# Kernel optimization log

Hardware: AMD Instinct MI355X
Metric: run time of the kernel (lower is better)

Reference implementation:

```python
import jax, jax.numpy as jnp
import numpy as np

BETA = 0.95
NUM_STEPS = 32


def setup_inputs() -> dict:
    key = jax.random.key(0)
    ks = jax.random.split(key, 6)
    B, IN, D, P = 1024, 512, 256, 8
    total = D * P
    x = jax.random.normal(ks[0], (B, IN), jnp.float32)
    W_proj = jax.random.normal(ks[1], (IN, total), jnp.float32) / np.sqrt(IN)
    b_proj = jnp.zeros((total,), jnp.float32)
    # uniform threshold distribution, sorted: linspace(0.5, 2.0, P)
    thresholds = jnp.linspace(0.5, 2.0, P, dtype=jnp.float32)
    rate_W = jax.random.normal(ks[2], (P, 1), jnp.float32) / np.sqrt(P)
    rate_b = jnp.zeros((1,), jnp.float32)
    conv1_w = jax.random.normal(ks[3], (P // 2, P, 3), jnp.float32) / np.sqrt(P * 3)
    conv1_b = jnp.zeros((P // 2,), jnp.float32)
    conv2_w = jax.random.normal(ks[4], (1, P // 2, 1), jnp.float32) / np.sqrt(P // 2)
    conv2_b = jnp.zeros((1,), jnp.float32)
    fusion = jnp.array([0.6, 0.4], jnp.float32)
    return dict(x=x, W_proj=W_proj, b_proj=b_proj, thresholds=thresholds,
                rate_W=rate_W, rate_b=rate_b, conv1_w=conv1_w, conv1_b=conv1_b,
                conv2_w=conv2_w, conv2_b=conv2_b, fusion=fusion)


def _conv1d(x, w, b):
    # x: [N, C_in, T], w: [C_out, C_in, K] -> [N, C_out, T] (SAME padding)
    y = jax.lax.conv_general_dilated(x, w, window_strides=(1,), padding='SAME',
                                     dimension_numbers=('NCH', 'OIH', 'NCH'))
    return y + b[None, :, None]


def reference(x, W_proj, b_proj, thresholds, rate_W, rate_b,
              conv1_w, conv1_b, conv2_w, conv2_b, fusion):
    B = x.shape[0]
    P = thresholds.shape[0]
    D = W_proj.shape[1] // P
    # constant input current per neuron: [B, D, P]
    I = (x @ W_proj + b_proj).reshape(B, D, P)

    # LIF recurrence (snntorch Leaky, reset_mechanism='subtract'):
    #   reset = H(mem_prev - thr); mem = beta*mem_prev + I - reset*thr; spk = H(mem - thr)
    def step(mem, _):
        reset = (mem > thresholds).astype(mem.dtype)
        mem = BETA * mem + I - reset * thresholds
        spk = (mem > thresholds).astype(mem.dtype)
        return mem, spk

    mem0 = jnp.zeros((B, D, P), x.dtype)
    _, spikes = jax.lax.scan(step, mem0, None, length=NUM_STEPS)  # [T, B, D, P]

    # rate branch
    rates = spikes.mean(axis=0)                        # [B, D, P]
    rate_dec = (rates @ rate_W)[..., 0] + rate_b[0]    # [B, D]

    # temporal branch: [B*D, P, T]
    s = jnp.transpose(spikes, (1, 2, 3, 0)).reshape(B * D, P, NUM_STEPS)
    h = jax.nn.relu(_conv1d(s, conv1_w, conv1_b))
    h = _conv1d(h, conv2_w, conv2_b)                   # [B*D, 1, T]
    temp_dec = h.mean(axis=-1).reshape(B, D)

    fw = jax.nn.softmax(fusion)
    return fw[0] * rate_dec + fw[1] * temp_dec
```

## Files before the change

### kernel.cpp

```cpp
#include <hip/hip_runtime.h>


constexpr int D_DIM   = 256;
constexpr int NTOT    = 2048;
constexpr int T_STEPS = 32;

typedef _Float16 f16x8 __attribute__((ext_vector_type(8)));
typedef float    f32x4 __attribute__((ext_vector_type(4)));
typedef ushort   ushort8 __attribute__((ext_vector_type(8)));

#define GLOBAL_AS __attribute__((address_space(1)))
#define LDS_AS    __attribute__((address_space(3)))

__device__ __forceinline__ void split_f16(float v, ushort& h, ushort& l) {
    const _Float16 hf = (_Float16)v;
    const _Float16 lf = (_Float16)((v - (float)hf) * 2048.0f);
    h = __builtin_bit_cast(ushort, hf);
    l = __builtin_bit_cast(ushort, lf);
}

__device__ __forceinline__ void conv_x_body(const float* __restrict__ x,
                                            ushort* __restrict__ Ah,
                                            ushort* __restrict__ Al,
                                            int blk, int t)
{
    const int idx = (blk * 256 + t) * 8;
    float v[8];
    *reinterpret_cast<float4*>(v)     = *reinterpret_cast<const float4*>(x + idx);
    *reinterpret_cast<float4*>(v + 4) = *reinterpret_cast<const float4*>(x + idx + 4);
    __align__(16) ushort h[8], l[8];
#pragma unroll
    for (int j = 0; j < 8; ++j) split_f16(v[j], h[j], l[j]);
    *reinterpret_cast<ushort8*>(Ah + idx) = *reinterpret_cast<const ushort8*>(h);
    *reinterpret_cast<ushort8*>(Al + idx) = *reinterpret_cast<const ushort8*>(l);
}

__device__ __forceinline__ void conv_w_body(const float* __restrict__ Wp,
                                            ushort* __restrict__ Bh,
                                            ushort* __restrict__ Bl,
                                            float (*tile)[69],
                                            int ib, int t)
{
    const int k0 = (ib >> 5) * 64;
    const int c0 = (ib & 31) * 64;
    {
        const int r = t >> 2, cq = (t & 3) * 16;
#pragma unroll
        for (int j = 0; j < 4; ++j)
            *reinterpret_cast<float4*>(&tile[r][cq + j * 4]) =
                *reinterpret_cast<const float4*>(Wp + (size_t)(k0 + r) * NTOT + c0 + cq + j * 4);
    }
    __syncthreads();
    const int rr = t >> 2, kc2 = (t & 3) * 16;
    __align__(16) ushort h[16], l[16];
#pragma unroll
    for (int j = 0; j < 16; ++j) split_f16(tile[kc2 + j][rr], h[j], l[j]);
    ushort* dh = Bh + (size_t)(c0 + rr) * 512 + k0 + kc2;
    ushort* dl = Bl + (size_t)(c0 + rr) * 512 + k0 + kc2;
    *reinterpret_cast<ushort8*>(dh)     = *reinterpret_cast<const ushort8*>(h);
    *reinterpret_cast<ushort8*>(dh + 8) = *reinterpret_cast<const ushort8*>(h + 8);
    *reinterpret_cast<ushort8*>(dl)     = *reinterpret_cast<const ushort8*>(l);
    *reinterpret_cast<ushort8*>(dl + 8) = *reinterpret_cast<const ushort8*>(l + 8);
}

__global__ __launch_bounds__(256)
void popcode_prep(const float* __restrict__ x, const float* __restrict__ Wp,
                  ushort* __restrict__ Ah, ushort* __restrict__ Al,
                  ushort* __restrict__ Bh, ushort* __restrict__ Bl)
{
    __shared__ float tile[64][69];
    const int t = threadIdx.x;
    if (blockIdx.x < 256) conv_x_body(x, Ah, Al, blockIdx.x, t);
    else                  conv_w_body(Wp, Bh, Bl, tile, blockIdx.x - 256, t);
}

__global__ __launch_bounds__(256)
void popcode_fused(const ushort* __restrict__ Ah_g, const ushort* __restrict__ Al_g,
                   const ushort* __restrict__ Bh_g, const ushort* __restrict__ Bl_g,
                   const float* __restrict__ bp, const float* __restrict__ thrs,
                   const float* __restrict__ rateW, const float* __restrict__ rateB,
                   const float* __restrict__ c1w, const float* __restrict__ c1b,
                   const float* __restrict__ c2w, const float* __restrict__ c2b,
                   const float* __restrict__ fus, float* __restrict__ out)
{
    __shared__ __align__(16) char smem[33664];
    LDS_AS char* lds0 = (LDS_AS char*)smem;

    const int tid  = threadIdx.x;
    const int w    = tid >> 6;
    const int lane = tid & 63;

    const int wg = ((blockIdx.x & 7) << 7) | (blockIdx.x >> 3);
    const int b0 = (wg & 15) * 64;
    const int c0 = (wg >> 4) * 32;

    const ushort* gbase = (w == 0) ? Ah_g : (w == 1) ? Al_g : (w == 2) ? Bh_g : Bl_g;
    const int     t0    = (w < 2) ? b0 : c0;
    const int     srow  = lane >> 2;
    const int     schk  = (lane & 3) * 8;
    const int     poff  = (w < 2) ? (w * 4096) : (8192 + (w - 2) * 2048);

    const int wr = (w >> 1) * 32;
    const int wc = (w & 1) * 16;
    const int lr = lane & 15;
    const int lg = lane >> 4;

    const f32x4 zero = {0.f, 0.f, 0.f, 0.f};
    f32x4 acch[2] = {zero, zero};
    f32x4 accl[2] = {zero, zero};

    auto stage = [&](int buf, int kt) {
        const int koff = kt * 32 + schk;
        const int base = buf * 12288 + poff;
        if (w < 2) {
#pragma unroll
            for (int i = 0; i < 4; ++i) {
                const ushort* src = gbase + (size_t)(t0 + srow + 16 * i) * 512 + koff;
                const int loff = __builtin_amdgcn_readfirstlane(base + i * 1024);
                __builtin_amdgcn_global_load_lds((const GLOBAL_AS uint*)src,
                                                 (LDS_AS uint*)(lds0 + loff), 16, 0, 0);
            }
        } else {
#pragma unroll
            for (int i = 0; i < 2; ++i) {
                const ushort* src = gbase + (size_t)(t0 + srow + 16 * i) * 512 + koff;
                const int loff = __builtin_amdgcn_readfirstlane(base + i * 1024);
                __builtin_amdgcn_global_load_lds((const GLOBAL_AS uint*)src,
                                                 (LDS_AS uint*)(lds0 + loff), 16, 0, 0);
            }
        }
    };

    auto compute = [&](int buf) {
        const int rbase = buf * 12288;
        f16x8 ah[2], al[2], bh, bl;
#pragma unroll
        for (int m = 0; m < 2; ++m) {
            const int row = wr + m * 16 + lr;
            ah[m] = *reinterpret_cast<const f16x8*>(smem + rbase +        row * 64 + lg * 16);
            al[m] = *reinterpret_cast<const f16x8*>(smem + rbase + 4096 + row * 64 + lg * 16);
        }
        {
            const int col = wc + lr;
            bh = *reinterpret_cast<const f16x8*>(smem + rbase +  8192 + col * 64 + lg * 16);
            bl = *reinterpret_cast<const f16x8*>(smem + rbase + 10240 + col * 64 + lg * 16);
        }
#pragma unroll
        for (int m = 0; m < 2; ++m) {
            acch[m] = __builtin_amdgcn_mfma_f32_16x16x32_f16(ah[m], bh, acch[m], 0, 0, 0);
            accl[m] = __builtin_amdgcn_mfma_f32_16x16x32_f16(al[m], bh, accl[m], 0, 0, 0);
            accl[m] = __builtin_amdgcn_mfma_f32_16x16x32_f16(ah[m], bl, accl[m], 0, 0, 0);
        }
    };

    float* wlds = (float*)(smem + 33280);
    if (tid < 96) wlds[tid] = c1w[tid];
    stage(0, 0);
    __syncthreads();

    for (int kt = 0; kt < 16; ++kt) {
        if (kt < 15) stage((kt + 1) & 1, kt + 1);
        compute(kt & 1);
        __syncthreads();
    }

    float* lutf = (float*)smem;
    for (int e = tid; e < 3072; e += 256) {
        const int k    = e >> 10;
        const int byte = (e >> 2) & 255;
        const int c    = e & 3;
        float v = (k == 1) ? c1b[c] : 0.f;
#pragma unroll
        for (int p = 0; p < 8; ++p)
            v = fmaf((float)((byte >> p) & 1), wlds[(c * 8 + p) * 3 + k], v);
        lutf[e] = v;
    }

    float* it = (float*)(smem + 24576);
    const float s = 1.0f / 2048.0f;
#pragma unroll
    for (int m = 0; m < 2; ++m)
#pragma unroll
        for (int v = 0; v < 4; ++v)
            it[(wr + m * 16 + lg * 4 + v) * 34 + wc + lr] =
                acch[m][v] + accl[m][v] * s;
    __syncthreads();

    const int row  = tid >> 2;
    const int dloc = tid & 3;
    const int dg   = (c0 >> 3) + dloc;

    const float* ip  = it + row * 34 + dloc * 8;
    float thrv[8];
#pragma unroll
    for (int p = 0; p < 8; ++p) thrv[p] = thrs[p];

    float Iv[8], mem[8];
    bool  spk[8];
    {
        const float4 bv0 = *reinterpret_cast<const float4*>(bp + dg * 8);
        const float4 bv1 = *reinterpret_cast<const float4*>(bp + dg * 8 + 4);
        Iv[0] = ip[0] + bv0.x; Iv[1] = ip[1] + bv0.y;
        Iv[2] = ip[2] + bv0.z; Iv[3] = ip[3] + bv0.w;
        Iv[4] = ip[4] + bv1.x; Iv[5] = ip[5] + bv1.y;
        Iv[6] = ip[6] + bv1.z; Iv[7] = ip[7] + bv1.w;
    }
#pragma unroll
    for (int p = 0; p < 8; ++p) { mem[p] = 0.f; spk[p] = false; }

    unsigned wrd[8] = {0u, 0u, 0u, 0u, 0u, 0u, 0u, 0u};
#pragma unroll
    for (int t = 0; t < T_STEPS; ++t) {
        unsigned by = 0u;
#pragma unroll
        for (int p = 0; p < 8; ++p) {
            const float m2 = fmaf(0.95f, mem[p], Iv[p]);
            mem[p] = spk[p] ? (m2 - thrv[p]) : m2;
            spk[p] = mem[p] > thrv[p];
            by |= spk[p] ? (1u << p) : 0u;
        }
        wrd[t >> 2] |= by << (8 * (t & 3));
    }

    float rsum = 0.f;
#pragma unroll
    for (int p = 0; p < 8; ++p) {
        const unsigned m = 0x01010101u << p;
        int cnt = 0;
#pragma unroll
        for (int q = 0; q < 8; ++q) cnt += __popc(wrd[q] & m);
        rsum = fmaf((float)cnt, rateW[p], rsum);
    }

    float w2c[4];
#pragma unroll
    for (int c = 0; c < 4; ++c) w2c[c] = c2w[c];
    auto getb = [&](int t) -> unsigned {
        return (wrd[t >> 2] >> (8 * (t & 3))) & 255u;
    };
    float tacc = 0.f;
    unsigned bprev = 0u;
    unsigned bcur  = getb(0);
#pragma unroll
    for (int t = 0; t < T_STEPS; ++t) {
        const unsigned bnext = (t < 31) ? getb(t + 1) : 0u;
        const float4 fa = *reinterpret_cast<const float4*>(lutf + bprev * 4);
        const float4 fb = *reinterpret_cast<const float4*>(lutf + 1024 + bcur * 4);
        const float4 fc = *reinterpret_cast<const float4*>(lutf + 2048 + bnext * 4);
        const float h0_ = (fa.x + fb.x) + fc.x;
        const float h1_ = (fa.y + fb.y) + fc.y;
        const float h2_ = (fa.z + fb.z) + fc.z;
        const float h3_ = (fa.w + fb.w) + fc.w;
        tacc = fmaf(fmaxf(h0_, 0.f), w2c[0], tacc);
        tacc = fmaf(fmaxf(h1_, 0.f), w2c[1], tacc);
        tacc = fmaf(fmaxf(h2_, 0.f), w2c[2], tacc);
        tacc = fmaf(fmaxf(h3_, 0.f), w2c[3], tacc);
        bprev = bcur;
        bcur  = bnext;
    }

    const float f0 = fus[0], f1 = fus[1];
    const float fm = fmaxf(f0, f1);
    const float e0 = __expf(f0 - fm), e1 = __expf(f1 - fm);
    const float inv = 1.f / (e0 + e1);

    const float rdec = rsum * (1.f / 32.f) + rateB[0];
    const float temp = tacc * (1.f / 32.f) + c2b[0];
    out[(b0 + row) * D_DIM + dg] = (e0 * inv) * rdec + (e1 * inv) * temp;
}

extern "C" void kernel_launch(void* const* d_in, const int* in_sizes, int n_in,
                              void* d_out, int out_size, void* d_ws, size_t ws_size,
                              hipStream_t stream) {
    const float* x     = (const float*)d_in[0];
    const float* Wp    = (const float*)d_in[1];
    const float* bp    = (const float*)d_in[2];
    const float* thrs  = (const float*)d_in[3];
    const float* rateW = (const float*)d_in[4];
    const float* rateB = (const float*)d_in[5];
    const float* c1w   = (const float*)d_in[6];
    const float* c1b   = (const float*)d_in[7];
    const float* c2w   = (const float*)d_in[8];
    const float* c2b   = (const float*)d_in[9];
    const float* fus   = (const float*)d_in[10];
    float* out = (float*)d_out;
    float* ws  = (float*)d_ws;

    ushort* Ah = reinterpret_cast<ushort*>(ws);
    ushort* Al = Ah + 1024 * 512;
    ushort* Bh = Al + 1024 * 512;
    ushort* Bl = Bh + 2048 * 512;

    popcode_prep<<<dim3(512), dim3(256), 0, stream>>>(x, Wp, Ah, Al, Bh, Bl);
    popcode_fused<<<dim3(1024), dim3(256), 0, stream>>>(
        Ah, Al, Bh, Bl, bp, thrs, rateW, rateB, c1w, c1b, c2w, c2b, fus, out);
}
```

Measured before the change: 122.3 us.

## Widen fused GEMM tile to 64x64 columns and halve workgroup count

Each workgroup now computes a 64x64 output tile instead of 64x32, so every wave does a 2x2 block of MFMAs and each A fragment loaded from LDS is reused across two B fragments. The staging layout changes to store MFMA-fragment-ordered chunks, so LDS reads become lane-contiguous. The LIF/decoder epilogue loops twice per thread to cover the wider tile. The grid halves to 512 blocks, which raises per-block LDS and register use and roughly doubles the serial epilogue per thread, at the cost of fewer workgroups to hide latency.

```diff
diff --git a/kernel.cpp b/kernel.cpp
--- a/kernel.cpp
+++ b/kernel.cpp
@@ -83,77 +83,68 @@
                    const float* __restrict__ c2w, const float* __restrict__ c2b,
                    const float* __restrict__ fus, float* __restrict__ out)
 {
-    __shared__ __align__(16) char smem[33664];
+    __shared__ __align__(16) char smem[49792];
     LDS_AS char* lds0 = (LDS_AS char*)smem;
 
     const int tid  = threadIdx.x;
     const int w    = tid >> 6;
     const int lane = tid & 63;
 
-    const int wg = ((blockIdx.x & 7) << 7) | (blockIdx.x >> 3);
+    const int wg = (blockIdx.x & 7) * 64 + (blockIdx.x >> 3);
     const int b0 = (wg & 15) * 64;
-    const int c0 = (wg >> 4) * 32;
+    const int c0 = (wg >> 4) * 64;
 
     const ushort* gbase = (w == 0) ? Ah_g : (w == 1) ? Al_g : (w == 2) ? Bh_g : Bl_g;
     const int     t0    = (w < 2) ? b0 : c0;
-    const int     srow  = lane >> 2;
-    const int     schk  = (lane & 3) * 8;
-    const int     poff  = (w < 2) ? (w * 4096) : (8192 + (w - 2) * 2048);
+    const int     srow  = lane & 15;
+    const int     schk  = (lane >> 4) * 8;
 
     const int wr = (w >> 1) * 32;
-    const int wc = (w & 1) * 16;
+    const int wc = (w & 1) * 32;
     const int lr = lane & 15;
     const int lg = lane >> 4;
 
     const f32x4 zero = {0.f, 0.f, 0.f, 0.f};
-    f32x4 acch[2] = {zero, zero};
-    f32x4 accl[2] = {zero, zero};
+    f32x4 acch[2][2] = {{zero, zero}, {zero, zero}};
+    f32x4 accl[2][2] = {{zero, zero}, {zero, zero}};
 
     auto stage = [&](int buf, int kt) {
         const int koff = kt * 32 + schk;
-        const int base = buf * 12288 + poff;
-        if (w < 2) {
-#pragma unroll
-            for (int i = 0; i < 4; ++i) {
-                const ushort* src = gbase + (size_t)(t0 + srow + 16 * i) * 512 + koff;
-                const int loff = __builtin_amdgcn_readfirstlane(base + i * 1024);
-                __builtin_amdgcn_global_load_lds((const GLOBAL_AS uint*)src,
-                                                 (LDS_AS uint*)(lds0 + loff), 16, 0, 0);
+#pragma unroll
+        for (int i = 0; i < 4; ++i) {
+            const ushort* src = gbase + (size_t)(t0 + srow + 16 * i) * 512 + koff;
+            const int loff = __builtin_amdgcn_readfirstlane(buf * 16384 + w * 4096 + i * 1024);
+            __builtin_amdgcn_global_load_lds((const GLOBAL_AS uint*)src,
+                                             (LDS_AS uint*)(lds0 + loff), 16, 0, 0);
+        }
+    };
+
+    auto compute = [&](int buf) {
+        const int rbase = buf * 16384 + lane * 16;
+        f16x8 ah[2], al[2], bh[2], bl[2];
+#pragma unroll
+        for (int m = 0; m < 2; ++m) {
+            const int qa = (w >> 1) * 2 + m;
+            ah[m] = *reinterpret_cast<const f16x8*>(smem + rbase +        qa * 1024);
+            al[m] = *reinterpret_cast<const f16x8*>(smem + rbase + 4096 + qa * 1024);
+        }
+#pragma unroll
+        for (int n = 0; n < 2; ++n) {
+            const int qb = (w & 1) * 2 + n;
+            bh[n] = *reinterpret_cast<const f16x8*>(smem + rbase +  8192 + qb * 1024);
+            bl[n] = *reinterpret_cast<const f16x8*>(smem + rbase + 12288 + qb * 1024);
+        }
+#pragma unroll
+        for (int m = 0; m < 2; ++m)
+#pragma unroll
+            for (int n = 0; n < 2; ++n) {
+                acch[m][n] = __builtin_amdgcn_mfma_f32_16x16x32_f16(ah[m], bh[n], acch[m][n], 0, 0, 0);
+                accl[m][n] = __builtin_amdgcn_mfma_f32_16x16x32_f16(al[m], bh[n], accl[m][n], 0, 0, 0);
+                accl[m][n] = __builtin_amdgcn_mfma_f32_16x16x32_f16(ah[m], bl[n], accl[m][n], 0, 0, 0);
             }
-        } else {
-#pragma unroll
-            for (int i = 0; i < 2; ++i) {
-                const ushort* src = gbase + (size_t)(t0 + srow + 16 * i) * 512 + koff;
-                const int loff = __builtin_amdgcn_readfirstlane(base + i * 1024);
-                __builtin_amdgcn_global_load_lds((const GLOBAL_AS uint*)src,
-                                                 (LDS_AS uint*)(lds0 + loff), 16, 0, 0);
-            }
-        }
     };
 
-    auto compute = [&](int buf) {
-        const int rbase = buf * 12288;
-        f16x8 ah[2], al[2], bh, bl;
-#pragma unroll
-        for (int m = 0; m < 2; ++m) {
-            const int row = wr + m * 16 + lr;
-            ah[m] = *reinterpret_cast<const f16x8*>(smem + rbase +        row * 64 + lg * 16);
-            al[m] = *reinterpret_cast<const f16x8*>(smem + rbase + 4096 + row * 64 + lg * 16);
-        }
-        {
-            const int col = wc + lr;
-            bh = *reinterpret_cast<const f16x8*>(smem + rbase +  8192 + col * 64 + lg * 16);
-            bl = *reinterpret_cast<const f16x8*>(smem + rbase + 10240 + col * 64 + lg * 16);
-        }
-#pragma unroll
-        for (int m = 0; m < 2; ++m) {
-            acch[m] = __builtin_amdgcn_mfma_f32_16x16x32_f16(ah[m], bh, acch[m], 0, 0, 0);
-            accl[m] = __builtin_amdgcn_mfma_f32_16x16x32_f16(al[m], bh, accl[m], 0, 0, 0);
-            accl[m] = __builtin_amdgcn_mfma_f32_16x16x32_f16(ah[m], bl, accl[m], 0, 0, 0);
-        }
-    };
-
-    float* wlds = (float*)(smem + 33280);
+    float* wlds = (float*)(smem + 49408);
     if (tid < 96) wlds[tid] = c1w[tid];
     stage(0, 0);
     __syncthreads();
@@ -176,97 +167,103 @@
         lutf[e] = v;
     }
 
-    float* it = (float*)(smem + 24576);
+    float* it = (float*)(smem + 32768);
     const float s = 1.0f / 2048.0f;
 #pragma unroll
     for (int m = 0; m < 2; ++m)
 #pragma unroll
-        for (int v = 0; v < 4; ++v)
-            it[(wr + m * 16 + lg * 4 + v) * 34 + wc + lr] =
-                acch[m][v] + accl[m][v] * s;
+        for (int n = 0; n < 2; ++n)
+#pragma unroll
+            for (int v = 0; v < 4; ++v)
+                it[(wr + m * 16 + lg * 4 + v) * 65 + wc + n * 16 + lr] =
+                    acch[m][n][v] + accl[m][n][v] * s;
     __syncthreads();
 
-    const int row  = tid >> 2;
-    const int dloc = tid & 3;
-    const int dg   = (c0 >> 3) + dloc;
-
-    const float* ip  = it + row * 34 + dloc * 8;
     float thrv[8];
 #pragma unroll
     for (int p = 0; p < 8; ++p) thrv[p] = thrs[p];
-
-    float Iv[8], mem[8];
-    bool  spk[8];
-    {
-        const float4 bv0 = *reinterpret_cast<const float4*>(bp + dg * 8);
-        const float4 bv1 = *reinterpret_cast<const float4*>(bp + dg * 8 + 4);
-        Iv[0] = ip[0] + bv0.x; Iv[1] = ip[1] + bv0.y;
-        Iv[2] = ip[2] + bv0.z; Iv[3] = ip[3] + bv0.w;
-        Iv[4] = ip[4] + bv1.x; Iv[5] = ip[5] + bv1.y;
-        Iv[6] = ip[6] + bv1.z; Iv[7] = ip[7] + bv1.w;
-    }
-#pragma unroll
-    for (int p = 0; p < 8; ++p) { mem[p] = 0.f; spk[p] = false; }
-
-    unsigned wrd[8] = {0u, 0u, 0u, 0u, 0u, 0u, 0u, 0u};
-#pragma unroll
-    for (int t = 0; t < T_STEPS; ++t) {
-        unsigned by = 0u;
-#pragma unroll
-        for (int p = 0; p < 8; ++p) {
-            const float m2 = fmaf(0.95f, mem[p], Iv[p]);
-            mem[p] = spk[p] ? (m2 - thrv[p]) : m2;
-            spk[p] = mem[p] > thrv[p];
-            by |= spk[p] ? (1u << p) : 0u;
-        }
-        wrd[t >> 2] |= by << (8 * (t & 3));
-    }
-
-    float rsum = 0.f;
-#pragma unroll
-    for (int p = 0; p < 8; ++p) {
-        const unsigned m = 0x01010101u << p;
-        int cnt = 0;
-#pragma unroll
-        for (int q = 0; q < 8; ++q) cnt += __popc(wrd[q] & m);
-        rsum = fmaf((float)cnt, rateW[p], rsum);
-    }
-
     float w2c[4];
 #pragma unroll
     for (int c = 0; c < 4; ++c) w2c[c] = c2w[c];
-    auto getb = [&](int t) -> unsigned {
-        return (wrd[t >> 2] >> (8 * (t & 3))) & 255u;
-    };
-    float tacc = 0.f;
-    unsigned bprev = 0u;
-    unsigned bcur  = getb(0);
-#pragma unroll
-    for (int t = 0; t < T_STEPS; ++t) {
-        const unsigned bnext = (t < 31) ? getb(t + 1) : 0u;
-        const float4 fa = *reinterpret_cast<const float4*>(lutf + bprev * 4);
-        const float4 fb = *reinterpret_cast<const float4*>(lutf + 1024 + bcur * 4);
-        const float4 fc = *reinterpret_cast<const float4*>(lutf + 2048 + bnext * 4);
-        const float h0_ = (fa.x + fb.x) + fc.x;
-        const float h1_ = (fa.y + fb.y) + fc.y;
-        const float h2_ = (fa.z + fb.z) + fc.z;
-        const float h3_ = (fa.w + fb.w) + fc.w;
-        tacc = fmaf(fmaxf(h0_, 0.f), w2c[0], tacc);
-        tacc = fmaf(fmaxf(h1_, 0.f), w2c[1], tacc);
-        tacc = fmaf(fmaxf(h2_, 0.f), w2c[2], tacc);
-        tacc = fmaf(fmaxf(h3_, 0.f), w2c[3], tacc);
-        bprev = bcur;
-        bcur  = bnext;
-    }
-
     const float f0 = fus[0], f1 = fus[1];
     const float fm = fmaxf(f0, f1);
     const float e0 = __expf(f0 - fm), e1 = __expf(f1 - fm);
     const float inv = 1.f / (e0 + e1);
-
-    const float rdec = rsum * (1.f / 32.f) + rateB[0];
-    const float temp = tacc * (1.f / 32.f) + c2b[0];
-    out[(b0 + row) * D_DIM + dg] = (e0 * inv) * rdec + (e1 * inv) * temp;
+    const float fw0 = e0 * inv, fw1 = e1 * inv;
+    const float rb_ = rateB[0];
+    const float bb2 = c2b[0];
+
+    const int row = tid >> 2;
+    for (int n2 = 0; n2 < 2; ++n2) {
+        const int dloc = (tid & 3) + n2 * 4;
+        const int dg   = (c0 >> 3) + dloc;
+
+        const float* ip = it + row * 65 + dloc * 8;
+        float Iv[8], mem[8];
+        bool  spk[8];
+        {
+            const float4 bv0 = *reinterpret_cast<const float4*>(bp + dg * 8);
+            const float4 bv1 = *reinterpret_cast<const float4*>(bp + dg * 8 + 4);
+            Iv[0] = ip[0] + bv0.x; Iv[1] = ip[1] + bv0.y;
+            Iv[2] = ip[2] + bv0.z; Iv[3] = ip[3] + bv0.w;
+            Iv[4] = ip[4] + bv1.x; Iv[5] = ip[5] + bv1.y;
+            Iv[6] = ip[6] + bv1.z; Iv[7] = ip[7] + bv1.w;
+        }
+#pragma unroll
+        for (int p = 0; p < 8; ++p) { mem[p] = 0.f; spk[p] = false; }
+
+        unsigned wrd[8] = {0u, 0u, 0u, 0u, 0u, 0u, 0u, 0u};
+#pragma unroll
+        for (int t = 0; t < T_STEPS; ++t) {
+            unsigned by = 0u;
+#pragma unroll
+            for (int p = 0; p < 8; ++p) {
+                const float m2 = fmaf(0.95f, mem[p], Iv[p]);
+                mem[p] = spk[p] ? (m2 - thrv[p]) : m2;
+                spk[p] = mem[p] > thrv[p];
+                by |= spk[p] ? (1u << p) : 0u;
+            }
+            wrd[t >> 2] |= by << (8 * (t & 3));
+        }
+
+        float rsum = 0.f;
+#pragma unroll
+        for (int p = 0; p < 8; ++p) {
+            const unsigned m = 0x01010101u << p;
+            int cnt = 0;
+#pragma unroll
+            for (int q = 0; q < 8; ++q) cnt += __popc(wrd[q] & m);
+            rsum = fmaf((float)cnt, rateW[p], rsum);
+        }
+
+        auto getb = [&](int t) -> unsigned {
+            return (wrd[t >> 2] >> (8 * (t & 3))) & 255u;
+        };
+        float tacc = 0.f;
+        unsigned bprev = 0u;
+        unsigned bcur  = getb(0);
+#pragma unroll
+        for (int t = 0; t < T_STEPS; ++t) {
+            const unsigned bnext = (t < 31) ? getb(t + 1) : 0u;
+            const float4 fa = *reinterpret_cast<const float4*>(lutf + bprev * 4);
+            const float4 fb = *reinterpret_cast<const float4*>(lutf + 1024 + bcur * 4);
+            const float4 fc = *reinterpret_cast<const float4*>(lutf + 2048 + bnext * 4);
+            const float h0_ = (fa.x + fb.x) + fc.x;
+            const float h1_ = (fa.y + fb.y) + fc.y;
+            const float h2_ = (fa.z + fb.z) + fc.z;
+            const float h3_ = (fa.w + fb.w) + fc.w;
+            tacc = fmaf(fmaxf(h0_, 0.f), w2c[0], tacc);
+            tacc = fmaf(fmaxf(h1_, 0.f), w2c[1], tacc);
+            tacc = fmaf(fmaxf(h2_, 0.f), w2c[2], tacc);
+            tacc = fmaf(fmaxf(h3_, 0.f), w2c[3], tacc);
+            bprev = bcur;
+            bcur  = bnext;
+        }
+
+        const float rdec = rsum * (1.f / 32.f) + rb_;
+        const float temp = tacc * (1.f / 32.f) + bb2;
+        out[(b0 + row) * D_DIM + dg] = fw0 * rdec + fw1 * temp;
+    }
 }
 
 extern "C" void kernel_launch(void* const* d_in, const int* in_sizes, int n_in,
@@ -292,6 +289,6 @@
     ushort* Bl = Bh + 2048 * 512;
 
     popcode_prep<<<dim3(512), dim3(256), 0, stream>>>(x, Wp, Ah, Al, Bh, Bl);
-    popcode_fused<<<dim3(1024), dim3(256), 0, stream>>>(
+    popcode_fused<<<dim3(512), dim3(256), 0, stream>>>(
         Ah, Al, Bh, Bl, bp, thrs, rateW, rateB, c1w, c1b, c2w, c2b, fus, out);
 }
```

Result: faster. 112.6 us (-7.9%).
